# Kernel optimization log

Measured on AMD Instinct MI355X. Metric: run time of the kernel, lower is better.

The kernel has to match this reference:

```python
import jax, jax.numpy as jnp
import numpy as np

N = 20000      # nodes
E = 320000     # edges
IN = 128       # in_channels
HID = 64       # hidden_channels (per-head out dim, concat=False -> mean over heads)
HEADS = 4
NEG_SLOPE = 0.2


def setup_inputs() -> dict:
    key = jax.random.key(0)
    ks = jax.random.split(key, 18)
    g = lambda i, shape: jax.random.normal(ks[i], shape, dtype=jnp.float32) * 0.05
    return {
        "x": jax.random.normal(ks[0], (N, IN), dtype=jnp.float32),
        "edge_index": jax.random.randint(ks[1], (2, E), 0, N),
        # GATConv params: lin weight (no bias in PyG lin), att_src/att_dst, out bias
        "W0": g(2, (IN, HEADS * HID)),
        "W1": g(3, (HID, HEADS * HID)),
        "W2": g(4, (HID, HEADS * HID)),
        "W3": g(5, (HID, HEADS * HID)),
        "a_src": g(6, (4, HEADS, HID)),
        "a_dst": g(7, (4, HEADS, HID)),
        "gat_b": g(8, (4, HID)),
        # residual projection for layer 0 (in_channels != hidden_channels)
        "res_W": g(9, (IN, HID)),
        "res_b": g(10, (HID,)),
        # edge classifier MLP: 2*HID -> HID -> HID -> 1
        "lin_W0": g(11, (2 * HID, HID)),
        "lin_b0": g(12, (HID,)),
        "lin_W1": g(13, (HID, HID)),
        "lin_b1": g(14, (HID,)),
        "lin_W2": g(15, (HID, 1)),
        "lin_b2": g(16, (1,)),
    }


def gat_conv(x, src, dst, W, asrc, adst, b, n):
    # x: [n, F_in]; src/dst: [E_tot] (self-loops included); W: [F_in, H*C]
    h = (x @ W).reshape(n, HEADS, HID)                     # [n, H, C]
    s_src = (h * asrc).sum(-1)                             # [n, H]
    s_dst = (h * adst).sum(-1)                             # [n, H]
    e = jax.nn.leaky_relu(s_src[src] + s_dst[dst], NEG_SLOPE)  # [E_tot, H]
    # segment softmax over incoming edges of each dst node
    m = jax.ops.segment_max(e, dst, num_segments=n)        # [n, H]
    p = jnp.exp(e - m[dst])
    z = jax.ops.segment_sum(p, dst, num_segments=n)
    alpha = p / z[dst]                                     # [E_tot, H]
    out = jax.ops.segment_sum(alpha[:, :, None] * h[src], dst, num_segments=n)  # [n, H, C]
    return out.mean(axis=1) + b                            # concat=False -> mean over heads


def reference(x, edge_index, W0, W1, W2, W3, a_src, a_dst, gat_b,
              res_W, res_b, lin_W0, lin_b0, lin_W1, lin_b1, lin_W2, lin_b2):
    n = x.shape[0]
    loop = jnp.arange(n)
    src = jnp.concatenate([edge_index[0], loop])  # PyG GATConv adds self-loops
    dst = jnp.concatenate([edge_index[1], loop])
    Ws = [W0, W1, W2, W3]
    h = x
    for i in range(4):
        h_prev = h
        h = gat_conv(h, src, dst, Ws[i], a_src[i], a_dst[i], gat_b[i], n)
        if i == 0:
            h = h + h_prev @ res_W + res_b   # projected residual
        else:
            h = h + h_prev
        h = jax.nn.elu(h)
    row, col = edge_index[0], edge_index[1]
    er = jnp.concatenate([h[row], h[col]], axis=1)        # [E, 2*HID]
    er = jax.nn.relu(er @ lin_W0 + lin_b0)                # shapes differ -> no residual
    er = jax.nn.relu(er @ lin_W1 + lin_b1 + er)           # shapes match -> residual
    logits = er @ lin_W2 + lin_b2                          # [E, 1]
    return logits
```

## Files before the change

### kernel.cpp

```cpp
#include <hip/hip_runtime.h>
#include <hip/hip_bf16.h>

#define NSLOPE 0.2f
#define MAXDEG 64

typedef short bf16x8 __attribute__((ext_vector_type(8)));
typedef float f32x4 __attribute__((ext_vector_type(4)));

__device__ __forceinline__ unsigned short f2b(float f) {
    unsigned u = __float_as_uint(f);
    unsigned r = (u + 0x7FFFu + ((u >> 16) & 1u)) >> 16;
    return (unsigned short)r;
}
__device__ __forceinline__ float b2f_lo(unsigned w) {
    return __uint_as_float(w << 16);
}
__device__ __forceinline__ float b2f_hi(unsigned w) {
    return __uint_as_float(w & 0xFFFF0000u);
}
__device__ __forceinline__ float b2f_s(short s) {
    return __uint_as_float(((unsigned)(unsigned short)s) << 16);
}
__device__ __forceinline__ unsigned packb(float lo, float hi) {
    return ((unsigned)f2b(hi) << 16) | (unsigned)f2b(lo);
}

__global__ __launch_bounds__(256) void prep_all(
    const float* __restrict__ W0, const float* __restrict__ W1,
    const float* __restrict__ W2, const float* __restrict__ W3,
    const float* __restrict__ resW, const float* __restrict__ linW0,
    const float* __restrict__ linW1, const float* __restrict__ linB0,
    const float* __restrict__ a_src, const float* __restrict__ a_dst,
    const float* __restrict__ gat_b, const float* __restrict__ res_b,
    short* __restrict__ WtC0e, short* __restrict__ WtC1,
    short* __restrict__ WtC2, short* __restrict__ WtC3,
    short* __restrict__ WtUV, short* __restrict__ WbT,
    float* __restrict__ wsd0, float* __restrict__ wsdL,
    float* __restrict__ bias128, float* __restrict__ gb0res,
    int* __restrict__ deg, int n) {
    const int bx = blockIdx.x;
    const int tid = threadIdx.x;
    if (bx == 0) {
        for (int idx = blockIdx.y * 256 + tid; idx < 64 * 640; idx += 256 * 16) {
            int j = idx / 640, k = idx - j * 640;
            float v;
            if (k < 512) {
                int h = k >> 7, kk = k & 127;
                v = W0[kk * 256 + h * 64 + j];
            } else {
                v = resW[(k - 512) * 64 + j];
            }
            WtC0e[idx] = (short)f2b(v);
        }
    } else if (bx <= 3) {
        const float* src = (bx == 1) ? W1 : (bx == 2) ? W2 : W3;
        short* dst = (bx == 1) ? WtC1 : (bx == 2) ? WtC2 : WtC3;
        for (int idx = blockIdx.y * 256 + tid; idx < 64 * 256; idx += 256 * 16) {
            int j = idx >> 8, rem = idx & 255;
            int h = rem >> 6, kk = rem & 63;
            dst[idx] = (short)f2b(src[kk * 256 + h * 64 + j]);
        }
    } else if (bx == 4) {
        if (blockIdx.y) return;
        for (int idx = tid; idx < 64 * 64; idx += 256) {
            int nn = idx >> 6, k = idx & 63;
            WtUV[idx] = (short)f2b(linW0[k * 64 + nn]);
        }
    } else if (bx == 5) {
        if (blockIdx.y) return;
        for (int idx = tid; idx < 64 * 64; idx += 256) {
            int nn = idx >> 6, k = idx & 63;
            WtUV[64 * 64 + idx] = (short)f2b(linW0[(k + 64) * 64 + nn]);
        }
    } else if (bx == 6) {
        if (blockIdx.y) return;
        for (int idx = tid; idx < 64 * 64; idx += 256) {
            int nn = idx >> 6, k = idx & 63;
            WbT[idx] = (short)f2b(linW1[k * 64 + nn]);
        }
    } else if (bx == 7) {
        if (blockIdx.y) return;
        if (tid < 128)
            bias128[tid] = (tid < 64) ? linB0[tid] : 0.f;
        else if (tid < 192)
            gb0res[tid - 128] = gat_b[tid - 128] + res_b[tid - 128];
    } else if (bx <= 11) {
        if (blockIdx.y) return;
        int l = bx - 8;
        const float* W = (l == 0) ? W0 : (l == 1) ? W1 : (l == 2) ? W2 : W3;
        const int K = (l == 0) ? 128 : 64;
        float* dst = (l == 0) ? wsd0 : wsdL + (l - 1) * 64 * 8;
        for (int idx = tid; idx < K * 8; idx += 256) {
            int k = idx >> 3, j = idx & 7, h = j & 3;
            const float* av = ((j < 4) ? a_src : a_dst) + l * 256 + h * 64;
            const float* wr = W + k * 256 + h * 64;
            float s = 0.f;
#pragma unroll 8
            for (int c = 0; c < 64; ++c) s += wr[c] * av[c];
            dst[k * 8 + j] = s;
        }
    } else {
        for (int i = blockIdx.y * 256 + tid; i < n; i += 256 * 16) deg[i] = 0;
    }
}

__global__ __launch_bounds__(256) void fill_convert(
    const int* __restrict__ ei, int* __restrict__ deg, int* __restrict__ csrS,
    int E, const float* __restrict__ x, const float* __restrict__ wsd0,
    unsigned* __restrict__ xb2, float* __restrict__ Ssrc,
    float* __restrict__ Sdst, int n, int eBlocks) {
    if ((int)blockIdx.x < eBlocks) {
        int e = blockIdx.x * 256 + threadIdx.x;
        if (e >= E) return;
        int s = ei[e], d = ei[E + e];
        int pos = atomicAdd(&deg[d], 1);
        if (pos < MAXDEG) csrS[d * MAXDEG + pos] = s;
        return;
    }
    const int nb = blockIdx.x - eBlocks;
    const int wid = threadIdx.x >> 6;
    const int lane = threadIdx.x & 63;
    const int node = nb * 4 + wid;
    if (node >= n) return;
    float2 xv = *(const float2*)&x[(size_t)node * 128 + lane * 2];
    xb2[(size_t)node * 64 + lane] = packb(xv.x, xv.y);
    float pv[8];
    const float* w0 = &wsd0[(lane * 2) * 8];
    const float* w1 = &wsd0[(lane * 2 + 1) * 8];
#pragma unroll
    for (int j = 0; j < 8; ++j) pv[j] = xv.x * w0[j] + xv.y * w1[j];
#pragma unroll
    for (int off = 1; off < 64; off <<= 1) {
#pragma unroll
        for (int j = 0; j < 8; ++j) pv[j] += __shfl_xor(pv[j], off, 64);
    }
    if (lane == 0) {
        *(float4*)&Ssrc[node * 4] = make_float4(pv[0], pv[1], pv[2], pv[3]);
        *(float4*)&Sdst[node * 4] = make_float4(pv[4], pv[5], pv[6], pv[7]);
    }
}

__global__ __launch_bounds__(256) void gat_gather128(
    const int* __restrict__ csrS, const int* __restrict__ deg,
    const float* __restrict__ Ssrc, const float* __restrict__ Sdst,
    const unsigned* __restrict__ xin, unsigned* __restrict__ aggB, int n) {
    __shared__ __align__(16) float qs[4][64][4];
    __shared__ int sjs[4][64];
    const int wid = threadIdx.x >> 6;
    const int lane = threadIdx.x & 63;
    const int node = blockIdx.x * 4 + wid;
    if (node >= n) return;
    const int dn = min(deg[node], MAXDEG);
    const int sreg = (lane < dn) ? csrS[node * MAXDEG + lane] : 0;
    const float4 sd = *(const float4*)&Sdst[node * 4];
    const float4 ss = *(const float4*)&Ssrc[node * 4];
    float c0 = ss.x + sd.x, c1 = ss.y + sd.y, c2 = ss.z + sd.z,
          c3 = ss.w + sd.w;
    c0 = c0 > 0.f ? c0 : NSLOPE * c0;
    c1 = c1 > 0.f ? c1 : NSLOPE * c1;
    c2 = c2 > 0.f ? c2 : NSLOPE * c2;
    c3 = c3 > 0.f ? c3 : NSLOPE * c3;
    float ps0 = __expf(c0), ps1 = __expf(c1), ps2 = __expf(c2),
          ps3 = __expf(c3);
    float4 sv = *(const float4*)&Ssrc[sreg * 4];
    float e0 = sv.x + sd.x, e1 = sv.y + sd.y;
    float e2 = sv.z + sd.z, e3 = sv.w + sd.w;
    e0 = e0 > 0.f ? e0 : NSLOPE * e0;
    e1 = e1 > 0.f ? e1 : NSLOPE * e1;
    e2 = e2 > 0.f ? e2 : NSLOPE * e2;
    e3 = e3 > 0.f ? e3 : NSLOPE * e3;
    const bool act = lane < dn;
    float q0 = act ? __expf(e0) : 0.f;
    float q1 = act ? __expf(e1) : 0.f;
    float q2 = act ? __expf(e2) : 0.f;
    float q3 = act ? __expf(e3) : 0.f;
    *(float4*)&qs[wid][lane][0] = make_float4(q0, q1, q2, q3);
    sjs[wid][lane] = sreg;
    float z0 = q0, z1 = q1, z2 = q2, z3 = q3;
#pragma unroll
    for (int off = 1; off < 64; off <<= 1) {
        z0 += __shfl_xor(z0, off, 64);
        z1 += __shfl_xor(z1, off, 64);
        z2 += __shfl_xor(z2, off, 64);
        z3 += __shfl_xor(z3, off, 64);
    }
    z0 += ps0; z1 += ps1; z2 += ps2; z3 += ps3;
    unsigned own = xin[(size_t)node * 64 + lane];
    float f0o = b2f_lo(own), f1o = b2f_hi(own);
    float u00 = ps0 * f0o, u01 = ps0 * f1o;
    float u10 = ps1 * f0o, u11 = ps1 * f1o;
    float u20 = ps2 * f0o, u21 = ps2 * f1o;
    float u30 = ps3 * f0o, u31 = ps3 * f1o;
#pragma unroll 4
    for (int p = 0; p < dn; ++p) {
        float4 qv = *(const float4*)&qs[wid][p][0];
        int sj = sjs[wid][p];
        unsigned fv = xin[(size_t)sj * 64 + lane];
        float f0 = b2f_lo(fv), f1 = b2f_hi(fv);
        u00 += qv.x * f0; u01 += qv.x * f1;
        u10 += qv.y * f0; u11 += qv.y * f1;
        u20 += qv.z * f0; u21 += qv.z * f1;
        u30 += qv.w * f0; u31 += qv.w * f1;
    }
    float i0 = 0.25f / z0, i1 = 0.25f / z1, i2 = 0.25f / z2, i3 = 0.25f / z3;
    size_t base = (size_t)node * 320;
    aggB[base + lane] = packb(u00 * i0, u01 * i0);
    aggB[base + 64 + lane] = packb(u10 * i1, u11 * i1);
    aggB[base + 128 + lane] = packb(u20 * i2, u21 * i2);
    aggB[base + 192 + lane] = packb(u30 * i3, u31 * i3);
    aggB[base + 256 + lane] = own;
}

__global__ __launch_bounds__(256) void gat_gather64(
    const int* __restrict__ csrS, const int* __restrict__ deg,
    const float* __restrict__ Ssrc, const float* __restrict__ Sdst,
    const unsigned* __restrict__ fin, unsigned* __restrict__ aggB, int n) {
    __shared__ __align__(16) float qs[4][64][4];
    __shared__ int sjs[4][64];
    const int wid = threadIdx.x >> 6;
    const int lane = threadIdx.x & 63;
    const int half = lane >> 5;
    const int cl = lane & 31;
    const int node = blockIdx.x * 4 + wid;
    if (node >= n) return;
    const int dn = min(deg[node], MAXDEG);
    const int sreg = (lane < dn) ? csrS[node * MAXDEG + lane] : 0;
    const float4 sd = *(const float4*)&Sdst[node * 4];
    const float4 ss = *(const float4*)&Ssrc[node * 4];
    float c0 = ss.x + sd.x, c1 = ss.y + sd.y, c2 = ss.z + sd.z,
          c3 = ss.w + sd.w;
    c0 = c0 > 0.f ? c0 : NSLOPE * c0;
    c1 = c1 > 0.f ? c1 : NSLOPE * c1;
    c2 = c2 > 0.f ? c2 : NSLOPE * c2;
    c3 = c3 > 0.f ? c3 : NSLOPE * c3;
    float ps0 = __expf(c0), ps1 = __expf(c1), ps2 = __expf(c2),
          ps3 = __expf(c3);
    float4 sv = *(const float4*)&Ssrc[sreg * 4];
    float e0 = sv.x + sd.x, e1 = sv.y + sd.y;
    float e2 = sv.z + sd.z, e3 = sv.w + sd.w;
    e0 = e0 > 0.f ? e0 : NSLOPE * e0;
    e1 = e1 > 0.f ? e1 : NSLOPE * e1;
    e2 = e2 > 0.f ? e2 : NSLOPE * e2;
    e3 = e3 > 0.f ? e3 : NSLOPE * e3;
    const bool act = lane < dn;
    float q0 = act ? __expf(e0) : 0.f;
    float q1 = act ? __expf(e1) : 0.f;
    float q2 = act ? __expf(e2) : 0.f;
    float q3 = act ? __expf(e3) : 0.f;
    *(float4*)&qs[wid][lane][0] = make_float4(q0, q1, q2, q3);
    sjs[wid][lane] = sreg;
    float z0 = q0, z1 = q1, z2 = q2, z3 = q3;
#pragma unroll
    for (int off = 1; off < 64; off <<= 1) {
        z0 += __shfl_xor(z0, off, 64);
        z1 += __shfl_xor(z1, off, 64);
        z2 += __shfl_xor(z2, off, 64);
        z3 += __shfl_xor(z3, off, 64);
    }
    z0 += ps0; z1 += ps1; z2 += ps2; z3 += ps3;
    unsigned own = fin[(size_t)node * 32 + cl];
    float u00 = 0.f, u01 = 0.f, u10 = 0.f, u11 = 0.f;
    float u20 = 0.f, u21 = 0.f, u30 = 0.f, u31 = 0.f;
#pragma unroll 4
    for (int p = half; p < dn; p += 2) {
        float4 qv = *(const float4*)&qs[wid][p][0];
        int sj = sjs[wid][p];
        unsigned fv = fin[(size_t)sj * 32 + cl];
        float f0 = b2f_lo(fv), f1 = b2f_hi(fv);
        u00 += qv.x * f0; u01 += qv.x * f1;
        u10 += qv.y * f0; u11 += qv.y * f1;
        u20 += qv.z * f0; u21 += qv.z * f1;
        u30 += qv.w * f0; u31 += qv.w * f1;
    }
    u00 += __shfl_xor(u00, 32, 64); u01 += __shfl_xor(u01, 32, 64);
    u10 += __shfl_xor(u10, 32, 64); u11 += __shfl_xor(u11, 32, 64);
    u20 += __shfl_xor(u20, 32, 64); u21 += __shfl_xor(u21, 32, 64);
    u30 += __shfl_xor(u30, 32, 64); u31 += __shfl_xor(u31, 32, 64);
    float f0o = b2f_lo(own), f1o = b2f_hi(own);
    u00 += ps0 * f0o; u01 += ps0 * f1o;
    u10 += ps1 * f0o; u11 += ps1 * f1o;
    u20 += ps2 * f0o; u21 += ps2 * f1o;
    u30 += ps3 * f0o; u31 += ps3 * f1o;
    float i0 = 0.25f / z0, i1 = 0.25f / z1;
    float i2 = 0.25f / z2, i3 = 0.25f / z3;
    size_t base = (size_t)node * 128;
    if (half == 0) {
        aggB[base + cl] = packb(u00 * i0, u01 * i0);
        aggB[base + 32 + cl] = packb(u10 * i1, u11 * i1);
    } else {
        aggB[base + 64 + cl] = packb(u20 * i2, u21 * i2);
        aggB[base + 96 + cl] = packb(u30 * i3, u31 * i3);
    }
}

template <int KK, bool SCORES>
__global__ __launch_bounds__(256) void gemm_layer(
    const short* __restrict__ Xb, const short* __restrict__ Wt,
    const float* __restrict__ gbias, const float* __restrict__ resid,
    const float* __restrict__ wsd, float* __restrict__ feat,
    short* __restrict__ featb, float* __restrict__ Ssrc,
    float* __restrict__ Sdst, int n) {
    __shared__ __align__(16) short Xs[64 * 136];
    __shared__ __align__(16) short Ws[4 * 64 * 40];
    const int tid = threadIdx.x;
    const int nb = blockIdx.x * 64;
    const int wid = tid >> 6;
    const int lane = tid & 63;
    const int t = lane & 15, quad = lane >> 4;
    f32x4 acc[4];
#pragma unroll
    for (int g = 0; g < 4; ++g) acc[g] = (f32x4){0.f, 0.f, 0.f, 0.f};
#pragma unroll 1
    for (int c0 = 0; c0 < KK / 128; ++c0) {
        __syncthreads();
        for (int idx = tid; idx < 1024; idx += 256) {
            int row = idx >> 4, c = idx & 15;
            uint4 v = make_uint4(0, 0, 0, 0);
            if (nb + row < n)
                v = *(const uint4*)(Xb + (size_t)(nb + row) * KK + c0 * 128 +
                                    c * 8);
            *(uint4*)(Xs + row * 136 + c * 8) = v;
        }
        for (int idx = tid; idx < 1024; idx += 256) {
            int kcs = idx >> 8, rem = idx & 255;
            int row = rem >> 2, c = rem & 3;
            *(uint4*)(Ws + kcs * 2560 + row * 40 + c * 8) =
                *(const uint4*)(Wt + (size_t)row * KK + c0 * 128 + kcs * 32 +
                                c * 8);
        }
        __syncthreads();
#pragma unroll
        for (int kc = 0; kc < 4; ++kc) {
            bf16x8 a =
                *(const bf16x8*)(Xs + (wid * 16 + t) * 136 + kc * 32 + quad * 8);
#pragma unroll
            for (int g = 0; g < 4; ++g) {
                bf16x8 b = *(const bf16x8*)(Ws + kc * 2560 + (g * 16 + t) * 40 +
                                            quad * 8);
                acc[g] =
                    __builtin_amdgcn_mfma_f32_16x16x32_bf16(a, b, acc[g], 0, 0, 0);
            }
        }
    }
    float bv[4];
#pragma unroll
    for (int g = 0; g < 4; ++g) bv[g] = gbias[g * 16 + t];
    float wsv[4][8];
    if (SCORES) {
#pragma unroll
        for (int g = 0; g < 4; ++g) {
            float4 lo = *(const float4*)&wsd[(g * 16 + t) * 8];
            float4 hi = *(const float4*)&wsd[(g * 16 + t) * 8 + 4];
            wsv[g][0] = lo.x; wsv[g][1] = lo.y; wsv[g][2] = lo.z;
            wsv[g][3] = lo.w; wsv[g][4] = hi.x; wsv[g][5] = hi.y;
            wsv[g][6] = hi.z; wsv[g][7] = hi.w;
        }
    }
#pragma unroll
    for (int r = 0; r < 4; ++r) {
        int node = nb + wid * 16 + quad * 4 + r;
        bool ok = node < n;
        float val[4];
#pragma unroll
        for (int g = 0; g < 4; ++g) {
            float v = acc[g][r] + bv[g];
            if (resid && ok) v += resid[(size_t)node * 64 + g * 16 + t];
            v = v > 0.f ? v : expm1f(v);
            val[g] = v;
            if (ok) {
                feat[(size_t)node * 64 + g * 16 + t] = v;
                featb[(size_t)node * 64 + g * 16 + t] = (short)f2b(v);
            }
        }
        if (SCORES) {
            float pv[8];
#pragma unroll
            for (int j = 0; j < 8; ++j) {
                pv[j] = val[0] * wsv[0][j] + val[1] * wsv[1][j] +
                        val[2] * wsv[2][j] + val[3] * wsv[3][j];
            }
#pragma unroll
            for (int off = 1; off < 16; off <<= 1) {
#pragma unroll
                for (int j = 0; j < 8; ++j) pv[j] += __shfl_xor(pv[j], off, 64);
            }
            if (t == 0 && ok) {
                *(float4*)&Ssrc[node * 4] =
                    make_float4(pv[0], pv[1], pv[2], pv[3]);
                *(float4*)&Sdst[node * 4] =
                    make_float4(pv[4], pv[5], pv[6], pv[7]);
            }
        }
    }
}

__global__ __launch_bounds__(256) void gemm_layer_uv(
    const short* __restrict__ Xb, const short* __restrict__ Wt,
    const float* __restrict__ gbias, const float* __restrict__ resid,
    const short* __restrict__ WtUV, const float* __restrict__ bias128,
    short* __restrict__ OutUV, int n) {
    constexpr int KK = 256;
    __shared__ __align__(16) short Xs[64 * 136];
    __shared__ __align__(16) short Ws[2 * 128 * 40];
    const int tid = threadIdx.x;
    const int nb = blockIdx.x * 64;
    const int wid = tid >> 6;
    const int lane = tid & 63;
    const int t = lane & 15, quad = lane >> 4;
    f32x4 acc[4];
#pragma unroll
    for (int g = 0; g < 4; ++g) acc[g] = (f32x4){0.f, 0.f, 0.f, 0.f};
#pragma unroll 1
    for (int c0 = 0; c0 < KK / 128; ++c0) {
        __syncthreads();
        for (int idx = tid; idx < 1024; idx += 256) {
            int row = idx >> 4, c = idx & 15;
            uint4 v = make_uint4(0, 0, 0, 0);
            if (nb + row < n)
                v = *(const uint4*)(Xb + (size_t)(nb + row) * KK + c0 * 128 +
                                    c * 8);
            *(uint4*)(Xs + row * 136 + c * 8) = v;
        }
        for (int idx = tid; idx < 1024; idx += 256) {
            int kcs = idx >> 8, rem = idx & 255;
            int row = rem >> 2, c = rem & 3;
            *(uint4*)(Ws + kcs * 2560 + row * 40 + c * 8) =
                *(const uint4*)(Wt + (size_t)row * KK + c0 * 128 + kcs * 32 +
                                c * 8);
        }
        __syncthreads();
#pragma unroll
        for (int kc = 0; kc < 4; ++kc) {
            bf16x8 a =
                *(const bf16x8*)(Xs + (wid * 16 + t) * 136 + kc * 32 + quad * 8);
#pragma unroll
            for (int g = 0; g < 4; ++g) {
                bf16x8 b = *(const bf16x8*)(Ws + kc * 2560 + (g * 16 + t) * 40 +
                                            quad * 8);
                acc[g] =
                    __builtin_amdgcn_mfma_f32_16x16x32_bf16(a, b, acc[g], 0, 0, 0);
            }
        }
    }
    float bv[4];
#pragma unroll
    for (int g = 0; g < 4; ++g) bv[g] = gbias[g * 16 + t];
    __syncthreads();
    for (int idx = tid; idx < 1024; idx += 256) {
        int kcs = idx >> 9, rem = idx & 511;
        int row = rem >> 2, c = rem & 3;
        *(uint4*)(Ws + kcs * 5120 + row * 40 + c * 8) =
            *(const uint4*)(WtUV + (size_t)row * 64 + kcs * 32 + c * 8);
    }
#pragma unroll
    for (int r = 0; r < 4; ++r) {
        int node = nb + wid * 16 + quad * 4 + r;
        bool ok = node < n;
        int lrow = wid * 16 + quad * 4 + r;
#pragma unroll
        for (int g = 0; g < 4; ++g) {
            float v = acc[g][r] + bv[g];
            if (ok) v += resid[(size_t)node * 64 + g * 16 + t];
            v = v > 0.f ? v : expm1f(v);
            Xs[lrow * 72 + g * 16 + t] = (short)f2b(v);
        }
    }
    __syncthreads();
    f32x4 acc2[8];
#pragma unroll
    for (int g = 0; g < 8; ++g) acc2[g] = (f32x4){0.f, 0.f, 0.f, 0.f};
#pragma unroll
    for (int kc = 0; kc < 2; ++kc) {
        bf16x8 a = *(const bf16x8*)(Xs + (wid * 16 + t) * 72 + kc * 32 + quad * 8);
#pragma unroll
        for (int g = 0; g < 8; ++g) {
            bf16x8 b = *(const bf16x8*)(Ws + kc * 5120 + (g * 16 + t) * 40 +
                                        quad * 8);
            acc2[g] = __builtin_amdgcn_mfma_f32_16x16x32_bf16(a, b, acc2[g], 0, 0, 0);
        }
    }
    float b2[8];
#pragma unroll
    for (int g = 0; g < 8; ++g) b2[g] = bias128[g * 16 + t];
#pragma unroll
    for (int r = 0; r < 4; ++r) {
        int node = nb + wid * 16 + quad * 4 + r;
        if (node >= n) continue;
#pragma unroll
        for (int g = 0; g < 8; ++g)
            OutUV[(size_t)node * 128 + g * 16 + t] =
                (short)f2b(acc2[g][r] + b2[g]);
    }
}

__global__ __launch_bounds__(256) void edge_mlp3(
    const int* __restrict__ ei, const unsigned* __restrict__ UV,
    const short* __restrict__ WbT, const float* __restrict__ bb,
    const float* __restrict__ Wc, const float* __restrict__ bc,
    float* __restrict__ out, int E) {
    __shared__ __align__(16) short t1b[64 * 72];
    __shared__ __align__(16) short wbs[64 * 72];
    const int tid = threadIdx.x;
    const int eBase = blockIdx.x * 64;
    for (int idx = tid; idx < 512; idx += 256) {
        int row = idx >> 3, c = idx & 7;
        *(uint4*)(wbs + row * 72 + c * 8) =
            *(const uint4*)(WbT + row * 64 + c * 8);
    }
    {
        const int j = tid & 31;
        const int eg = tid >> 5;
        int rr[8], cc[8];
#pragma unroll
        for (int it = 0; it < 8; ++it) {
            int e = eBase + it * 8 + eg;
            rr[it] = (e < E) ? ei[e] : 0;
            cc[it] = (e < E) ? ei[E + e] : 0;
        }
#pragma unroll
        for (int it = 0; it < 8; ++it) {
            unsigned uu = UV[(size_t)rr[it] * 64 + j];
            unsigned vv = UV[(size_t)cc[it] * 64 + 32 + j];
            float lo = fmaxf(b2f_lo(uu) + b2f_lo(vv), 0.f);
            float hi = fmaxf(b2f_hi(uu) + b2f_hi(vv), 0.f);
            *(unsigned*)(t1b + (it * 8 + eg) * 72 + j * 2) = packb(lo, hi);
        }
    }
    __syncthreads();
    const int w = tid >> 6, lane = tid & 63;
    const int t = lane & 15, quad = lane >> 4;
    f32x4 acc[4];
#pragma unroll
    for (int g = 0; g < 4; ++g) acc[g] = (f32x4){0.f, 0.f, 0.f, 0.f};
#pragma unroll
    for (int kc = 0; kc < 2; ++kc) {
        bf16x8 a = *(const bf16x8*)(t1b + (w * 16 + t) * 72 + kc * 32 + quad * 8);
#pragma unroll
        for (int g = 0; g < 4; ++g) {
            bf16x8 b = *(const bf16x8*)(wbs + (g * 16 + t) * 72 + kc * 32 + quad * 8);
            acc[g] = __builtin_amdgcn_mfma_f32_16x16x32_bf16(a, b, acc[g], 0, 0, 0);
        }
    }
    float wcv[4], bbv[4];
#pragma unroll
    for (int g = 0; g < 4; ++g) {
        wcv[g] = Wc[g * 16 + t];
        bbv[g] = bb[g * 16 + t];
    }
    const float bcv = bc[0];
#pragma unroll
    for (int r = 0; r < 4; ++r) {
        int el = w * 16 + quad * 4 + r;
        float part = 0.f;
#pragma unroll
        for (int g = 0; g < 4; ++g) {
            float t1v = b2f_s(t1b[el * 72 + g * 16 + t]);
            float t2 = fmaxf(acc[g][r] + bbv[g] + t1v, 0.f);
            part += t2 * wcv[g];
        }
        part += __shfl_xor(part, 1, 64);
        part += __shfl_xor(part, 2, 64);
        part += __shfl_xor(part, 4, 64);
        part += __shfl_xor(part, 8, 64);
        int e = eBase + el;
        if (t == 0 && e < E) out[e] = part + bcv;
    }
}

extern "C" void kernel_launch(void* const* d_in, const int* in_sizes, int n_in,
                              void* d_out, int out_size, void* d_ws,
                              size_t ws_size, hipStream_t stream) {
    const float* x = (const float*)d_in[0];
    const int* ei = (const int*)d_in[1];
    const float* W0 = (const float*)d_in[2];
    const float* W1 = (const float*)d_in[3];
    const float* W2 = (const float*)d_in[4];
    const float* W3 = (const float*)d_in[5];
    const float* a_src = (const float*)d_in[6];
    const float* a_dst = (const float*)d_in[7];
    const float* gat_b = (const float*)d_in[8];
    const float* res_W = (const float*)d_in[9];
    const float* res_b = (const float*)d_in[10];
    const float* lin_W0 = (const float*)d_in[11];
    const float* lin_b0 = (const float*)d_in[12];
    const float* lin_W1 = (const float*)d_in[13];
    const float* lin_b1 = (const float*)d_in[14];
    const float* lin_W2 = (const float*)d_in[15];
    const float* lin_b2 = (const float*)d_in[16];
    float* out = (float*)d_out;

    const int N = in_sizes[0] / 128;
    const int E = in_sizes[1] / 2;

    char* ws = (char*)d_ws;
    unsigned* aggB = (unsigned*)ws;
    float* featA = (float*)(aggB + (size_t)N * 320);
    float* featB = featA + (size_t)N * 64;
    unsigned* xb2 = (unsigned*)(featB + (size_t)N * 64);
    unsigned* featbA = xb2 + (size_t)N * 64;
    unsigned* featbB = featbA + (size_t)N * 32;
    unsigned* UVb = featbB + (size_t)N * 32;
    float* Ssrc = (float*)(UVb + (size_t)N * 64);
    float* Sdst = Ssrc + (size_t)N * 4;
    short* WtC0e = (short*)(Sdst + (size_t)N * 4);
    short* WtC1 = WtC0e + 64 * 640;
    short* WtC2 = WtC1 + 64 * 256;
    short* WtC3 = WtC2 + 64 * 256;
    short* WtUV = WtC3 + 64 * 256;
    short* WbT = WtUV + 128 * 64;
    float* wsd0 = (float*)(WbT + 64 * 64);
    float* wsdL = wsd0 + 128 * 8;
    float* bias128 = wsdL + 3 * 64 * 8;
    float* gb0res = bias128 + 128;
    int* deg = (int*)(gb0res + 64);
    int* csrS = deg + N;

    const int gemmBlocks = (N + 63) / 64;
    const int eBlocks = (E + 255) / 256;
    const int nodeW = (N + 3) / 4;

    prep_all<<<dim3(13, 16), 256, 0, stream>>>(
        W0, W1, W2, W3, res_W, lin_W0, lin_W1, lin_b0, a_src, a_dst, gat_b,
        res_b, WtC0e, WtC1, WtC2, WtC3, WtUV, WbT, wsd0, wsdL, bias128,
        gb0res, deg, N);
    fill_convert<<<eBlocks + nodeW, 256, 0, stream>>>(
        ei, deg, csrS, E, x, wsd0, xb2, Ssrc, Sdst, N, eBlocks);

    gat_gather128<<<nodeW, 256, 0, stream>>>(csrS, deg, Ssrc, Sdst, xb2, aggB,
                                             N);
    gemm_layer<640, true><<<gemmBlocks, 256, 0, stream>>>(
        (const short*)aggB, WtC0e, gb0res, nullptr, wsdL, featA,
        (short*)featbA, Ssrc, Sdst, N);

    gat_gather64<<<nodeW, 256, 0, stream>>>(csrS, deg, Ssrc, Sdst, featbA,
                                            aggB, N);
    gemm_layer<256, true><<<gemmBlocks, 256, 0, stream>>>(
        (const short*)aggB, WtC1, gat_b + 64, featA, wsdL + 64 * 8, featB,
        (short*)featbB, Ssrc, Sdst, N);
    gat_gather64<<<nodeW, 256, 0, stream>>>(csrS, deg, Ssrc, Sdst, featbB,
                                            aggB, N);
    gemm_layer<256, true><<<gemmBlocks, 256, 0, stream>>>(
        (const short*)aggB, WtC2, gat_b + 128, featB, wsdL + 2 * 64 * 8,
        featA, (short*)featbA, Ssrc, Sdst, N);

    gat_gather64<<<nodeW, 256, 0, stream>>>(csrS, deg, Ssrc, Sdst, featbA,
                                            aggB, N);
    gemm_layer_uv<<<gemmBlocks, 256, 0, stream>>>(
        (const short*)aggB, WtC3, gat_b + 192, featA, WtUV, bias128,
        (short*)UVb, N);

    edge_mlp3<<<(E + 63) / 64, 256, 0, stream>>>(ei, UVb, WbT, lin_b1, lin_W2,
                                                 lin_b2, out, E);
}
```

Before: 290.4 us.

## Read residual input directly in layer-0 GEMM and move weight transposes into fill kernel

The layer-0 gather no longer copies each node's own bf16 input row into the aggregation buffer; the layer-0 GEMM instead reads the last K-chunk straight from the bf16 input array through a second pointer. This removes one write and one read of N×128 bf16 per call. Separately, the weight transpose and bf16 conversion work moves out of the prep kernel into extra blocks of the fill/convert kernel, so the prep kernel only zeroes degrees and computes the small score vectors. The result is a shorter serial prep launch, at the cost of a more heterogeneous fill kernel.

```diff
diff --git a/kernel.cpp b/kernel.cpp
--- a/kernel.cpp
+++ b/kernel.cpp
@@ -25,74 +25,36 @@
     return ((unsigned)f2b(hi) << 16) | (unsigned)f2b(lo);
 }
 
-__global__ __launch_bounds__(256) void prep_all(
+__global__ __launch_bounds__(256) void prep_small(
     const float* __restrict__ W0, const float* __restrict__ W1,
     const float* __restrict__ W2, const float* __restrict__ W3,
-    const float* __restrict__ resW, const float* __restrict__ linW0,
-    const float* __restrict__ linW1, const float* __restrict__ linB0,
     const float* __restrict__ a_src, const float* __restrict__ a_dst,
     const float* __restrict__ gat_b, const float* __restrict__ res_b,
-    short* __restrict__ WtC0e, short* __restrict__ WtC1,
-    short* __restrict__ WtC2, short* __restrict__ WtC3,
-    short* __restrict__ WtUV, short* __restrict__ WbT,
-    float* __restrict__ wsd0, float* __restrict__ wsdL,
-    float* __restrict__ bias128, float* __restrict__ gb0res,
-    int* __restrict__ deg, int n) {
+    const float* __restrict__ linB0, float* __restrict__ wsd0,
+    float* __restrict__ wsdL, float* __restrict__ bias128,
+    float* __restrict__ gb0res, int* __restrict__ deg, int n) {
     const int bx = blockIdx.x;
     const int tid = threadIdx.x;
-    if (bx == 0) {
-        for (int idx = blockIdx.y * 256 + tid; idx < 64 * 640; idx += 256 * 16) {
-            int j = idx / 640, k = idx - j * 640;
-            float v;
-            if (k < 512) {
-                int h = k >> 7, kk = k & 127;
-                v = W0[kk * 256 + h * 64 + j];
-            } else {
-                v = resW[(k - 512) * 64 + j];
-            }
-            WtC0e[idx] = (short)f2b(v);
-        }
-    } else if (bx <= 3) {
-        const float* src = (bx == 1) ? W1 : (bx == 2) ? W2 : W3;
-        short* dst = (bx == 1) ? WtC1 : (bx == 2) ? WtC2 : WtC3;
-        for (int idx = blockIdx.y * 256 + tid; idx < 64 * 256; idx += 256 * 16) {
-            int j = idx >> 8, rem = idx & 255;
-            int h = rem >> 6, kk = rem & 63;
-            dst[idx] = (short)f2b(src[kk * 256 + h * 64 + j]);
-        }
-    } else if (bx == 4) {
-        if (blockIdx.y) return;
-        for (int idx = tid; idx < 64 * 64; idx += 256) {
-            int nn = idx >> 6, k = idx & 63;
-            WtUV[idx] = (short)f2b(linW0[k * 64 + nn]);
-        }
-    } else if (bx == 5) {
-        if (blockIdx.y) return;
-        for (int idx = tid; idx < 64 * 64; idx += 256) {
-            int nn = idx >> 6, k = idx & 63;
-            WtUV[64 * 64 + idx] = (short)f2b(linW0[(k + 64) * 64 + nn]);
-        }
-    } else if (bx == 6) {
-        if (blockIdx.y) return;
-        for (int idx = tid; idx < 64 * 64; idx += 256) {
-            int nn = idx >> 6, k = idx & 63;
-            WbT[idx] = (short)f2b(linW1[k * 64 + nn]);
-        }
-    } else if (bx == 7) {
-        if (blockIdx.y) return;
-        if (tid < 128)
-            bias128[tid] = (tid < 64) ? linB0[tid] : 0.f;
-        else if (tid < 192)
-            gb0res[tid - 128] = gat_b[tid - 128] + res_b[tid - 128];
-    } else if (bx <= 11) {
-        if (blockIdx.y) return;
-        int l = bx - 8;
-        const float* W = (l == 0) ? W0 : (l == 1) ? W1 : (l == 2) ? W2 : W3;
-        const int K = (l == 0) ? 128 : 64;
-        float* dst = (l == 0) ? wsd0 : wsdL + (l - 1) * 64 * 8;
-        for (int idx = tid; idx < K * 8; idx += 256) {
+    if (bx < 40) {
+        for (int i = bx * 256 + tid; i < n; i += 40 * 256) deg[i] = 0;
+    } else if (bx == 40) {
+        for (int idx = tid; idx < 128 * 8; idx += 256) {
             int k = idx >> 3, j = idx & 7, h = j & 3;
-            const float* av = ((j < 4) ? a_src : a_dst) + l * 256 + h * 64;
+            const float* av = ((j < 4) ? a_src : a_dst) + h * 64;
+            const float* wr = W0 + k * 256 + h * 64;
+            float s = 0.f;
+#pragma unroll 8
+            for (int c = 0; c < 64; ++c) s += wr[c] * av[c];
+            wsd0[k * 8 + j] = s;
+        }
+    } else if (bx <= 43) {
+        int l = bx - 41;
+        const float* W = (l == 0) ? W1 : (l == 1) ? W2 : W3;
+        float* dst = wsdL + l * 64 * 8;
+        for (int idx = tid; idx < 64 * 8; idx += 256) {
+            int k = idx >> 3, j = idx & 7, h = j & 3;
+            const float* av =
+                ((j < 4) ? a_src : a_dst) + (l + 1) * 256 + h * 64;
             const float* wr = W + k * 256 + h * 64;
             float s = 0.f;
 #pragma unroll 8
@@ -100,7 +62,10 @@
             dst[k * 8 + j] = s;
         }
     } else {
-        for (int i = blockIdx.y * 256 + tid; i < n; i += 256 * 16) deg[i] = 0;
+        if (tid < 128)
+            bias128[tid] = (tid < 64) ? linB0[tid] : 0.f;
+        else if (tid < 192)
+            gb0res[tid - 128] = gat_b[tid - 128] + res_b[tid - 128];
     }
 }
 
@@ -108,18 +73,69 @@
     const int* __restrict__ ei, int* __restrict__ deg, int* __restrict__ csrS,
     int E, const float* __restrict__ x, const float* __restrict__ wsd0,
     unsigned* __restrict__ xb2, float* __restrict__ Ssrc,
-    float* __restrict__ Sdst, int n, int eBlocks) {
-    if ((int)blockIdx.x < eBlocks) {
-        int e = blockIdx.x * 256 + threadIdx.x;
+    float* __restrict__ Sdst, int n, int eBlocks,
+    const float* __restrict__ W0, const float* __restrict__ W1,
+    const float* __restrict__ W2, const float* __restrict__ W3,
+    const float* __restrict__ resW, const float* __restrict__ linW0,
+    const float* __restrict__ linW1, short* __restrict__ WtC0e,
+    short* __restrict__ WtC1, short* __restrict__ WtC2,
+    short* __restrict__ WtC3, short* __restrict__ WtUV,
+    short* __restrict__ WbT) {
+    const int tid = threadIdx.x;
+    constexpr int TB = 38;
+    if ((int)blockIdx.x < TB) {
+        const int bx = blockIdx.x;
+        if (bx < 16) {
+            for (int idx = bx * 256 + tid; idx < 64 * 640; idx += 16 * 256) {
+                int j = idx / 640, k = idx - j * 640;
+                float v;
+                if (k < 512) {
+                    int h = k >> 7, kk = k & 127;
+                    v = W0[kk * 256 + h * 64 + j];
+                } else {
+                    v = resW[(k - 512) * 64 + j];
+                }
+                WtC0e[idx] = (short)f2b(v);
+            }
+        } else if (bx < 32) {
+            for (int idx = (bx - 16) * 256 + tid; idx < 3 * 64 * 256;
+                 idx += 16 * 256) {
+                int w = idx >> 14, rem = idx & 16383;
+                const float* src = (w == 0) ? W1 : (w == 1) ? W2 : W3;
+                short* dst = (w == 0) ? WtC1 : (w == 1) ? WtC2 : WtC3;
+                int j = rem >> 8, r2 = rem & 255;
+                int h = r2 >> 6, kk = r2 & 63;
+                dst[rem] = (short)f2b(src[kk * 256 + h * 64 + j]);
+            }
+        } else if (bx < 36) {
+            for (int idx = (bx - 32) * 256 + tid; idx < 2 * 64 * 64;
+                 idx += 4 * 256) {
+                int half = idx >> 12, r2 = idx & 4095;
+                int nn = r2 >> 6, k = r2 & 63;
+                WtUV[half * 4096 + r2] =
+                    (short)f2b(linW0[(k + half * 64) * 64 + nn]);
+            }
+        } else {
+            for (int idx = (bx - 36) * 256 + tid; idx < 64 * 64;
+                 idx += 2 * 256) {
+                int nn = idx >> 6, k = idx & 63;
+                WbT[idx] = (short)f2b(linW1[k * 64 + nn]);
+            }
+        }
+        return;
+    }
+    const int bxe = (int)blockIdx.x - TB;
+    if (bxe < eBlocks) {
+        int e = bxe * 256 + tid;
         if (e >= E) return;
         int s = ei[e], d = ei[E + e];
         int pos = atomicAdd(&deg[d], 1);
         if (pos < MAXDEG) csrS[d * MAXDEG + pos] = s;
         return;
     }
-    const int nb = blockIdx.x - eBlocks;
-    const int wid = threadIdx.x >> 6;
-    const int lane = threadIdx.x & 63;
+    const int nb = bxe - eBlocks;
+    const int wid = tid >> 6;
+    const int lane = tid & 63;
     const int node = nb * 4 + wid;
     if (node >= n) return;
     float2 xv = *(const float2*)&x[(size_t)node * 128 + lane * 2];
@@ -203,12 +219,11 @@
         u30 += qv.w * f0; u31 += qv.w * f1;
     }
     float i0 = 0.25f / z0, i1 = 0.25f / z1, i2 = 0.25f / z2, i3 = 0.25f / z3;
-    size_t base = (size_t)node * 320;
+    size_t base = (size_t)node * 256;
     aggB[base + lane] = packb(u00 * i0, u01 * i0);
     aggB[base + 64 + lane] = packb(u10 * i1, u11 * i1);
     aggB[base + 128 + lane] = packb(u20 * i2, u21 * i2);
     aggB[base + 192 + lane] = packb(u30 * i3, u31 * i3);
-    aggB[base + 256 + lane] = own;
 }
 
 __global__ __launch_bounds__(256) void gat_gather64(
@@ -293,13 +308,13 @@
     }
 }
 
-template <int KK, bool SCORES>
+template <int KK, int KA, bool SCORES>
 __global__ __launch_bounds__(256) void gemm_layer(
-    const short* __restrict__ Xb, const short* __restrict__ Wt,
-    const float* __restrict__ gbias, const float* __restrict__ resid,
-    const float* __restrict__ wsd, float* __restrict__ feat,
-    short* __restrict__ featb, float* __restrict__ Ssrc,
-    float* __restrict__ Sdst, int n) {
+    const short* __restrict__ Xb, const short* __restrict__ XbR,
+    const short* __restrict__ Wt, const float* __restrict__ gbias,
+    const float* __restrict__ resid, const float* __restrict__ wsd,
+    float* __restrict__ feat, short* __restrict__ featb,
+    float* __restrict__ Ssrc, float* __restrict__ Sdst, int n) {
     __shared__ __align__(16) short Xs[64 * 136];
     __shared__ __align__(16) short Ws[4 * 64 * 40];
     const int tid = threadIdx.x;
@@ -316,9 +331,13 @@
         for (int idx = tid; idx < 1024; idx += 256) {
             int row = idx >> 4, c = idx & 15;
             uint4 v = make_uint4(0, 0, 0, 0);
-            if (nb + row < n)
-                v = *(const uint4*)(Xb + (size_t)(nb + row) * KK + c0 * 128 +
-                                    c * 8);
+            if (nb + row < n) {
+                if (c0 * 128 < KA)
+                    v = *(const uint4*)(Xb + (size_t)(nb + row) * KA +
+                                        c0 * 128 + c * 8);
+                else
+                    v = *(const uint4*)(XbR + (size_t)(nb + row) * 128 + c * 8);
+            }
             *(uint4*)(Xs + row * 136 + c * 8) = v;
         }
         for (int idx = tid; idx < 1024; idx += 256) {
@@ -618,30 +637,31 @@
     const int gemmBlocks = (N + 63) / 64;
     const int eBlocks = (E + 255) / 256;
     const int nodeW = (N + 3) / 4;
-
-    prep_all<<<dim3(13, 16), 256, 0, stream>>>(
-        W0, W1, W2, W3, res_W, lin_W0, lin_W1, lin_b0, a_src, a_dst, gat_b,
-        res_b, WtC0e, WtC1, WtC2, WtC3, WtUV, WbT, wsd0, wsdL, bias128,
-        gb0res, deg, N);
-    fill_convert<<<eBlocks + nodeW, 256, 0, stream>>>(
-        ei, deg, csrS, E, x, wsd0, xb2, Ssrc, Sdst, N, eBlocks);
+    const int tBlocks = 38;
+
+    prep_small<<<45, 256, 0, stream>>>(W0, W1, W2, W3, a_src, a_dst, gat_b,
+                                       res_b, lin_b0, wsd0, wsdL, bias128,
+                                       gb0res, deg, N);
+    fill_convert<<<tBlocks + eBlocks + nodeW, 256, 0, stream>>>(
+        ei, deg, csrS, E, x, wsd0, xb2, Ssrc, Sdst, N, eBlocks, W0, W1, W2,
+        W3, res_W, lin_W0, lin_W1, WtC0e, WtC1, WtC2, WtC3, WtUV, WbT);
 
     gat_gather128<<<nodeW, 256, 0, stream>>>(csrS, deg, Ssrc, Sdst, xb2, aggB,
                                              N);
-    gemm_layer<640, true><<<gemmBlocks, 256, 0, stream>>>(
-        (const short*)aggB, WtC0e, gb0res, nullptr, wsdL, featA,
-        (short*)featbA, Ssrc, Sdst, N);
+    gemm_layer<640, 512, true><<<gemmBlocks, 256, 0, stream>>>(
+        (const short*)aggB, (const short*)xb2, WtC0e, gb0res, nullptr, wsdL,
+        featA, (short*)featbA, Ssrc, Sdst, N);
 
     gat_gather64<<<nodeW, 256, 0, stream>>>(csrS, deg, Ssrc, Sdst, featbA,
                                             aggB, N);
-    gemm_layer<256, true><<<gemmBlocks, 256, 0, stream>>>(
-        (const short*)aggB, WtC1, gat_b + 64, featA, wsdL + 64 * 8, featB,
-        (short*)featbB, Ssrc, Sdst, N);
+    gemm_layer<256, 256, true><<<gemmBlocks, 256, 0, stream>>>(
+        (const short*)aggB, nullptr, WtC1, gat_b + 64, featA, wsdL + 64 * 8,
+        featB, (short*)featbB, Ssrc, Sdst, N);
     gat_gather64<<<nodeW, 256, 0, stream>>>(csrS, deg, Ssrc, Sdst, featbB,
                                             aggB, N);
-    gemm_layer<256, true><<<gemmBlocks, 256, 0, stream>>>(
-        (const short*)aggB, WtC2, gat_b + 128, featB, wsdL + 2 * 64 * 8,
-        featA, (short*)featbA, Ssrc, Sdst, N);
+    gemm_layer<256, 256, true><<<gemmBlocks, 256, 0, stream>>>(
+        (const short*)aggB, nullptr, WtC2, gat_b + 128, featB,
+        wsdL + 2 * 64 * 8, featA, (short*)featbA, Ssrc, Sdst, N);
 
     gat_gather64<<<nodeW, 256, 0, stream>>>(csrS, deg, Ssrc, Sdst, featbA,
                                             aggB, N);
```

New measurement: 290.7 us. Within noise of the previous version (+0.1%).
